# Kernel optimization log

Measured on AMD Instinct MI355X. Metric: run time of the kernel, lower is better.

Reference implementation:

```python
import jax, jax.numpy as jnp
import numpy as np

T, B, D = 2048, 16, 1024
INIT_K_BIAS = -2.0


def setup_inputs() -> dict:
    key = jax.random.key(0)
    k1, k2, k3 = jax.random.split(key, 3)
    xavier = (6.0 / (D + D)) ** 0.5  # xavier_uniform bound for [D, D]
    x = jax.random.normal(k1, (T, B, D), dtype=jnp.float32)
    h0 = jnp.zeros((B, D), dtype=jnp.float32)
    W_k = jax.random.uniform(k2, (D, D), dtype=jnp.float32, minval=-xavier, maxval=xavier)
    b_k = jnp.full((D,), INIT_K_BIAS, dtype=jnp.float32)
    W_v = jax.random.uniform(k3, (D, D), dtype=jnp.float32, minval=-xavier, maxval=xavier)
    b_v = jnp.zeros((D,), dtype=jnp.float32)
    return {"x": x, "h0": h0, "W_k": W_k, "b_k": b_k, "W_v": W_v, "b_v": b_v}


def reference(x, h0, W_k, b_k, W_v, b_v):
    # Batched gate/value projections: x @ W^T + b, over all T*B positions at once.
    k_all = jax.nn.sigmoid(jnp.einsum('tbd,ed->tbe', x, W_k) + b_k)  # [T,B,D]
    v_all = jnp.tanh(jnp.einsum('tbd,ed->tbe', x, W_v) + b_v)        # [T,B,D]

    def step(h_prev, kv):
        k_t, v_t = kv
        h_new = (1.0 - k_t) * h_prev + k_t * v_t
        return h_new, h_new

    _, hs = jax.lax.scan(step, h0, (k_all, v_all))  # hs: [T,B,D]
    h = jnp.concatenate([h0[None], hs], axis=0)      # [T+1,B,D]
    output = hs * jax.nn.silu(hs)                    # [T,B,D]
    return output, h
```

## Files before the change

kernel.cpp:

```cpp
#include <hip/hip_runtime.h>
#include <hip/hip_bf16.h>
#include <stdint.h>
#include <stddef.h>

#define T_DIM 2048
#define B_DIM 16
#define D_DIM 1024
#define BD    (B_DIM * D_DIM)
#define TBD   ((size_t)T_DIM * BD)

using bf16 = __hip_bfloat16;
typedef __attribute__((ext_vector_type(8))) short short8;
typedef __attribute__((ext_vector_type(4))) float f32x4;

__device__ __forceinline__ unsigned f2bf(float f) {
    unsigned u = __float_as_uint(f);
    return (u + 0x7FFFu + ((u >> 16) & 1u)) >> 16;
}

__global__ __launch_bounds__(256) void cvt_f32_bf16(
    const float* __restrict__ src, short* __restrict__ dst, int n8)
{
    int i = blockIdx.x * 256 + threadIdx.x;
    if (i >= n8) return;
    const float* p = src + (size_t)i * 8;
    f32x4 a = *(const f32x4*)p;
    f32x4 b = *(const f32x4*)(p + 4);
    short8 r;
    r[0] = (short)f2bf(a[0]); r[1] = (short)f2bf(a[1]);
    r[2] = (short)f2bf(a[2]); r[3] = (short)f2bf(a[3]);
    r[4] = (short)f2bf(b[0]); r[5] = (short)f2bf(b[1]);
    r[6] = (short)f2bf(b[2]); r[7] = (short)f2bf(b[3]);
    *(short8*)(dst + (size_t)i * 8) = r;
}

typedef __attribute__((address_space(1))) void gvoid;
typedef __attribute__((address_space(3))) void lvoid;
__device__ __forceinline__ void gload_lds16(const short* g, short* l) {
    __builtin_amdgcn_global_load_lds((gvoid*)g, (lvoid*)l, 16, 0, 0);
}

__global__ __launch_bounds__(256, 4) void gemm_kv_bf16(
    const short* __restrict__ xb,
    const short* __restrict__ Wkb, const float* __restrict__ bk,
    const short* __restrict__ Wvb, const float* __restrict__ bv,
    float* __restrict__ kout, float* __restrict__ vout)
{
    __shared__ short sA[2][128 * 32];
    __shared__ short sB[2][128 * 32];

    const int tid  = threadIdx.x;
    const int lane = tid & 63;
    const int wave = tid >> 6;
    const int wm   = wave & 1;
    const int wn   = wave >> 1;
    const int quad = lane >> 4;
    const int l15  = lane & 15;

    const int lin = blockIdx.x + (blockIdx.y << 3) + (blockIdx.z << 11);
    const int swz = ((lin & 7) << 9) | (lin >> 3);
    const bool is_k = (swz >> 11) == 0;
    const int blkm = (swz >> 3) & 255;
    const int blkn = swz & 7;

    const short* W    = is_k ? Wkb : Wvb;
    const float* bias = is_k ? bk : bv;
    float*       outp = is_k ? kout : vout;

    const int m0 = blkm * 128;
    const int n0 = blkn * 128;

    const int srow = wave * 16 + (lane >> 2);
    const int skof = (lane & 3) * 8;
    const short* ga = xb + (size_t)(m0 + srow) * D_DIM + skof;
    const short* gb = W  + (size_t)(n0 + srow) * D_DIM + skof;
    const int lofs = wave * 512;

    auto STAGE = [&](int buf, int ks) {
        const size_t ko = (size_t)ks * 32;
        gload_lds16(ga + ko,                        &sA[buf][lofs]);
        gload_lds16(ga + ko + (size_t)64 * D_DIM,   &sA[buf][2048 + lofs]);
        gload_lds16(gb + ko,                        &sB[buf][lofs]);
        gload_lds16(gb + ko + (size_t)64 * D_DIM,   &sB[buf][2048 + lofs]);
    };

    f32x4 acc[4][4] = {};

    STAGE(0, 0);
    int cur = 0;
    for (int ks = 0; ks < D_DIM / 32; ++ks) {
        __syncthreads();
        if (ks + 1 < D_DIM / 32) STAGE(cur ^ 1, ks + 1);

        const short* lA = sA[cur];
        const short* lB = sB[cur];
        short8 a[4], b[4];
#pragma unroll
        for (int mt = 0; mt < 4; ++mt)
            a[mt] = *(const short8*)&lA[(wm * 64 + mt * 16 + l15) * 32 + quad * 8];
#pragma unroll
        for (int nt = 0; nt < 4; ++nt)
            b[nt] = *(const short8*)&lB[(wn * 64 + nt * 16 + l15) * 32 + quad * 8];
#pragma unroll
        for (int mt = 0; mt < 4; ++mt)
#pragma unroll
            for (int nt = 0; nt < 4; ++nt)
                acc[mt][nt] = __builtin_amdgcn_mfma_f32_16x16x32_bf16(
                    a[mt], b[nt], acc[mt][nt], 0, 0, 0);
        cur ^= 1;
    }

    const int gm0 = blkm * 128 + wm * 64 + quad * 4;
    const int gn  = blkn * 128 + wn * 64 + l15;
#pragma unroll
    for (int nt = 0; nt < 4; ++nt) {
        const int n = gn + nt * 16;
        const float bs = bias[n];
#pragma unroll
        for (int mt = 0; mt < 4; ++mt) {
            const int m = gm0 + mt * 16;
#pragma unroll
            for (int r = 0; r < 4; ++r) {
                float pre = acc[mt][nt][r] + bs;
                pre = fminf(20.f, fmaxf(-20.f, pre));
                float o;
                if (is_k) o = 1.f / (1.f + __expf(-pre));
                else      o = 2.f / (1.f + __expf(-2.f * pre)) - 1.f;
                outp[(size_t)(m + r) * D_DIM + n] = o;
            }
        }
    }
}

__device__ __forceinline__ short8 load_cvt8(const float* p) {
    f32x4 a = *(const f32x4*)p;
    f32x4 b = *(const f32x4*)(p + 4);
    short8 r;
    r[0] = (short)f2bf(a[0]); r[1] = (short)f2bf(a[1]);
    r[2] = (short)f2bf(a[2]); r[3] = (short)f2bf(a[3]);
    r[4] = (short)f2bf(b[0]); r[5] = (short)f2bf(b[1]);
    r[6] = (short)f2bf(b[2]); r[7] = (short)f2bf(b[3]);
    return r;
}

__global__ __launch_bounds__(256) void gemm_kv_f32src(
    const float* __restrict__ x,
    const float* __restrict__ Wk, const float* __restrict__ bk,
    const float* __restrict__ Wv, const float* __restrict__ bv,
    float* __restrict__ kout, float* __restrict__ vout)
{
    const int tid  = threadIdx.x;
    const int lane = tid & 63;
    const int wave = tid >> 6;
    const int wm   = wave & 1;
    const int wn   = wave >> 1;
    const int quad = lane >> 4;
    const int l15  = lane & 15;

    const int blkn = blockIdx.x;
    const int blkm = blockIdx.y;
    const bool is_k = (blockIdx.z == 0);

    const float* W    = is_k ? Wk : Wv;
    const float* bias = is_k ? bk : bv;
    float*       outp = is_k ? kout : vout;

    const int m0 = blkm * 128 + wm * 64;
    const int n0 = blkn * 128 + wn * 64;

    const float* ap = x + (size_t)(m0 + l15) * D_DIM + quad * 8;
    const float* bp = W + (size_t)(n0 + l15) * D_DIM + quad * 8;

    f32x4 acc[4][4] = {};

    for (int ks = 0; ks < D_DIM / 32; ++ks) {
        short8 a[4], b[4];
#pragma unroll
        for (int mt = 0; mt < 4; ++mt)
            a[mt] = load_cvt8(ap + (size_t)mt * 16 * D_DIM + ks * 32);
#pragma unroll
        for (int nt = 0; nt < 4; ++nt)
            b[nt] = load_cvt8(bp + (size_t)nt * 16 * D_DIM + ks * 32);
#pragma unroll
        for (int mt = 0; mt < 4; ++mt)
#pragma unroll
            for (int nt = 0; nt < 4; ++nt)
                acc[mt][nt] = __builtin_amdgcn_mfma_f32_16x16x32_bf16(
                    a[mt], b[nt], acc[mt][nt], 0, 0, 0);
    }

    const int gm0 = blkm * 128 + wm * 64 + quad * 4;
    const int gn  = blkn * 128 + wn * 64 + l15;
#pragma unroll
    for (int nt = 0; nt < 4; ++nt) {
        const int n = gn + nt * 16;
        const float bs = bias[n];
#pragma unroll
        for (int mt = 0; mt < 4; ++mt) {
            const int m = gm0 + mt * 16;
#pragma unroll
            for (int r = 0; r < 4; ++r) {
                float pre = acc[mt][nt][r] + bs;
                pre = fminf(20.f, fmaxf(-20.f, pre));
                float o;
                if (is_k) o = 1.f / (1.f + __expf(-pre));
                else      o = 2.f / (1.f + __expf(-2.f * pre)) - 1.f;
                outp[(size_t)(m + r) * D_DIM + n] = o;
            }
        }
    }
}

__global__ __launch_bounds__(256) void scan_phase_a(
    const float* kw, const float* vw,
    float* __restrict__ Aab, float* __restrict__ Bab, int tc)
{
    const int bd = blockIdx.x * 256 + threadIdx.x;
    const int c  = blockIdx.y;
    const float* kp = kw + (size_t)c * tc * BD + bd;
    const float* vp = vw + (size_t)c * tc * BD + bd;

    float A = 1.f, Bv = 0.f;
    for (int t0 = 0; t0 < tc; t0 += 16) {
        float kk[16], vv[16];
#pragma unroll
        for (int j = 0; j < 16; ++j) {
            kk[j] = kp[(size_t)(t0 + j) * BD];
            vv[j] = vp[(size_t)(t0 + j) * BD];
        }
#pragma unroll
        for (int j = 0; j < 16; ++j) {
            const float a = 1.f - kk[j];
            A  = A * a;
            Bv = a * Bv + kk[j] * vv[j];
        }
    }
    Aab[(size_t)c * BD + bd] = A;
    Bab[(size_t)c * BD + bd] = Bv;
}

__global__ __launch_bounds__(256) void scan_phase_b(
    const float* __restrict__ h0,
    const float* __restrict__ Aab, const float* __restrict__ Bab,
    float* __restrict__ Hinit, float* hsec, int nc)
{
    const int bd = blockIdx.x * 256 + threadIdx.x;
    float h = h0[bd];
    hsec[bd] = h;
    for (int c0 = 0; c0 < nc; c0 += 16) {
        float aa[16], bb[16];
#pragma unroll
        for (int j = 0; j < 16; ++j) {
            aa[j] = Aab[(size_t)(c0 + j) * BD + bd];
            bb[j] = Bab[(size_t)(c0 + j) * BD + bd];
        }
#pragma unroll
        for (int j = 0; j < 16; ++j) {
            Hinit[(size_t)(c0 + j) * BD + bd] = h;
            h = aa[j] * h + bb[j];
        }
    }
}

__global__ __launch_bounds__(256) void scan_phase_c(
    const float* kw, const float* vw, const float* __restrict__ Hinit,
    float* outp, float* hsec, int tc)
{
    const int bd = blockIdx.x * 256 + threadIdx.x;
    const int c  = blockIdx.y;
    float h = Hinit[(size_t)c * BD + bd];

    const size_t base = (size_t)c * tc * BD + bd;
    const float* kp = kw + base;
    const float* vp = vw + base;
    float* op = outp + base;
    float* hp = hsec + base + BD;

    float kk[16], vv[16];
#pragma unroll
    for (int j = 0; j < 16; ++j) {
        kk[j] = kp[(size_t)j * BD];
        vv[j] = vp[(size_t)j * BD];
    }
    for (int t0 = 0; t0 < tc; t0 += 16) {
        float kn[16], vn[16];
        if (t0 + 16 < tc) {
#pragma unroll
            for (int j = 0; j < 16; ++j) {
                kn[j] = kp[(size_t)(t0 + 16 + j) * BD];
                vn[j] = vp[(size_t)(t0 + 16 + j) * BD];
            }
        }
#pragma unroll
        for (int j = 0; j < 16; ++j) {
            h = (1.f - kk[j]) * h + kk[j] * vv[j];
            hp[(size_t)(t0 + j) * BD] = h;
            const float sig = 1.f / (1.f + __expf(-h));
            op[(size_t)(t0 + j) * BD] = h * h * sig;
        }
        if (t0 + 16 < tc) {
#pragma unroll
            for (int j = 0; j < 16; ++j) { kk[j] = kn[j]; vv[j] = vn[j]; }
        }
    }
}

__global__ __launch_bounds__(64) void scan_kernel(
    const float* kw, const float* vw, const float* h0,
    float* outp, float* hsec)
{
    const int c = blockIdx.x * 64 + threadIdx.x;
    float h = h0[c];
    hsec[c] = h;

    const float* kp = kw + c;
    const float* vp = vw + c;
    float* op = outp + c;
    float* hp = hsec + BD + c;

    for (int t = 0; t < T_DIM; t += 8) {
        float kk[8], vv[8];
#pragma unroll
        for (int j = 0; j < 8; ++j) {
            kk[j] = kp[(size_t)(t + j) * BD];
            vv[j] = vp[(size_t)(t + j) * BD];
        }
#pragma unroll
        for (int j = 0; j < 8; ++j) {
            h = (1.f - kk[j]) * h + kk[j] * vv[j];
            hp[(size_t)(t + j) * BD] = h;
            const float sig = 1.f / (1.f + __expf(-h));
            op[(size_t)(t + j) * BD] = h * h * sig;
        }
    }
}

extern "C" void kernel_launch(void* const* d_in, const int* in_sizes, int n_in,
                              void* d_out, int out_size, void* d_ws, size_t ws_size,
                              hipStream_t stream)
{
    const float* x  = (const float*)d_in[0];
    const float* h0 = (const float*)d_in[1];
    const float* Wk = (const float*)d_in[2];
    const float* bk = (const float*)d_in[3];
    const float* Wv = (const float*)d_in[4];
    const float* bv = (const float*)d_in[5];

    float* outp = (float*)d_out;
    float* hsec = outp + TBD;

    float* kw = outp;
    float* vw = hsec + BD;

    const size_t bf16_bytes = (TBD + 2 * (size_t)D_DIM * D_DIM) * sizeof(short);

    bool bf16_path = false;
    size_t avail = ws_size;
    char* scan_ws = (char*)d_ws;
    if (ws_size >= bf16_bytes) {
        bf16_path = true;
        avail   -= bf16_bytes;
        scan_ws += bf16_bytes;
    }

    int nc = 0;
    if (avail >= 3 * (size_t)128 * BD * sizeof(float))      nc = 128;
    else if (avail >= 3 * (size_t)32 * BD * sizeof(float))  nc = 32;
    const int tc = nc ? T_DIM / nc : 0;

    float* Aab   = nc ? (float*)scan_ws : nullptr;
    float* Bab   = nc ? Aab + (size_t)nc * BD : nullptr;
    float* Hinit = nc ? Bab + (size_t)nc * BD : nullptr;

    if (bf16_path) {
        short* xb  = (short*)d_ws;
        short* Wkb = xb + TBD;
        short* Wvb = Wkb + (size_t)D_DIM * D_DIM;
        cvt_f32_bf16<<<dim3((int)(TBD / 8 / 256)), 256, 0, stream>>>(x, xb, (int)(TBD / 8));
        cvt_f32_bf16<<<dim3(D_DIM * D_DIM / 8 / 256), 256, 0, stream>>>(Wk, Wkb, D_DIM * D_DIM / 8);
        cvt_f32_bf16<<<dim3(D_DIM * D_DIM / 8 / 256), 256, 0, stream>>>(Wv, Wvb, D_DIM * D_DIM / 8);
        gemm_kv_bf16<<<dim3(8, 256, 2), 256, 0, stream>>>(xb, Wkb, bk, Wvb, bv, kw, vw);
    } else {
        gemm_kv_f32src<<<dim3(8, 256, 2), 256, 0, stream>>>(x, Wk, bk, Wv, bv, kw, vw);
    }

    if (nc) {
        scan_phase_a<<<dim3(BD / 256, nc), 256, 0, stream>>>(kw, vw, Aab, Bab, tc);
        scan_phase_b<<<dim3(BD / 256), 256, 0, stream>>>(h0, Aab, Bab, Hinit, hsec, nc);
        scan_phase_c<<<dim3(BD / 256, nc), 256, 0, stream>>>(kw, vw, Hinit, outp, hsec, tc);
    } else {
        scan_kernel<<<dim3(BD / 64), 64, 0, stream>>>(kw, vw, h0, outp, hsec);
    }
}
```

Baseline: 702.8 us.

## Fuse K/V GEMMs and compute per-tile scan aggregates in GEMM epilogue

Adds a fused GEMM kernel that computes both the K and V projections per tile, sharing the x tile loads. Its epilogue also reduces each 8-timestep block into (A,B) affine scan aggregates. This removes the separate scan phase A pass that re-read all of k and v from memory, and halves the x reads. A short sequential kernel turns the 256 aggregates into initial states, and a parallel apply kernel produces h and the output. The cost is twice the accumulators per block, so the launch bound drops to 2 blocks per CU and occupancy is lower. The old phase_c prefetch was also simplified.

```diff
diff --git a/kernel.cpp b/kernel.cpp
--- a/kernel.cpp
+++ b/kernel.cpp
@@ -8,6 +8,8 @@
 #define D_DIM 1024
 #define BD    (B_DIM * D_DIM)
 #define TBD   ((size_t)T_DIM * BD)
+#define NG    256
+#define TG    8
 
 using bf16 = __hip_bfloat16;
 typedef __attribute__((ext_vector_type(8))) short short8;
@@ -40,14 +42,25 @@
     __builtin_amdgcn_global_load_lds((gvoid*)g, (lvoid*)l, 16, 0, 0);
 }
 
-__global__ __launch_bounds__(256, 4) void gemm_kv_bf16(
+__device__ __forceinline__ float sigm(float x) {
+    x = fminf(20.f, fmaxf(-20.f, x));
+    return 1.f / (1.f + __expf(-x));
+}
+__device__ __forceinline__ float tanh_(float x) {
+    x = fminf(20.f, fmaxf(-20.f, x));
+    return 2.f / (1.f + __expf(-2.f * x)) - 1.f;
+}
+
+__global__ __launch_bounds__(256, 2) void gemm_kv_fused(
     const short* __restrict__ xb,
     const short* __restrict__ Wkb, const float* __restrict__ bk,
     const short* __restrict__ Wvb, const float* __restrict__ bv,
-    float* __restrict__ kout, float* __restrict__ vout)
+    float* __restrict__ kout, float* __restrict__ vout,
+    float2* __restrict__ agg)
 {
     __shared__ short sA[2][128 * 32];
-    __shared__ short sB[2][128 * 32];
+    __shared__ short sBk[2][128 * 32];
+    __shared__ short sBv[2][128 * 32];
 
     const int tid  = threadIdx.x;
     const int lane = tid & 63;
@@ -57,6 +70,132 @@
     const int quad = lane >> 4;
     const int l15  = lane & 15;
 
+    const int lin = blockIdx.x + (blockIdx.y << 3);
+    const int swz = ((lin & 7) << 8) | (lin >> 3);
+    const int blkm = swz >> 3;
+    const int blkn = swz & 7;
+
+    const int m0 = blkm * 128;
+    const int n0 = blkn * 128;
+
+    const int srow = wave * 16 + (lane >> 2);
+    const int skof = (lane & 3) * 8;
+    const short* ga = xb  + (size_t)(m0 + srow) * D_DIM + skof;
+    const short* gk = Wkb + (size_t)(n0 + srow) * D_DIM + skof;
+    const short* gv = Wvb + (size_t)(n0 + srow) * D_DIM + skof;
+    const int lofs = wave * 512;
+
+    auto STAGE = [&](int buf, int ks) {
+        const size_t ko = (size_t)ks * 32;
+        gload_lds16(ga + ko,                        &sA[buf][lofs]);
+        gload_lds16(ga + ko + (size_t)64 * D_DIM,   &sA[buf][2048 + lofs]);
+        gload_lds16(gk + ko,                        &sBk[buf][lofs]);
+        gload_lds16(gk + ko + (size_t)64 * D_DIM,   &sBk[buf][2048 + lofs]);
+        gload_lds16(gv + ko,                        &sBv[buf][lofs]);
+        gload_lds16(gv + ko + (size_t)64 * D_DIM,   &sBv[buf][2048 + lofs]);
+    };
+
+    f32x4 ack[4][4] = {};
+    f32x4 acv[4][4] = {};
+
+    STAGE(0, 0);
+    int cur = 0;
+    for (int ks = 0; ks < D_DIM / 32; ++ks) {
+        __syncthreads();
+        if (ks + 1 < D_DIM / 32) STAGE(cur ^ 1, ks + 1);
+
+        const short* lA = sA[cur];
+        const short* lK = sBk[cur];
+        const short* lV = sBv[cur];
+        short8 a[4], bkf[4], bvf[4];
+#pragma unroll
+        for (int mt = 0; mt < 4; ++mt)
+            a[mt] = *(const short8*)&lA[(wm * 64 + mt * 16 + l15) * 32 + quad * 8];
+#pragma unroll
+        for (int nt = 0; nt < 4; ++nt) {
+            bkf[nt] = *(const short8*)&lK[(wn * 64 + nt * 16 + l15) * 32 + quad * 8];
+            bvf[nt] = *(const short8*)&lV[(wn * 64 + nt * 16 + l15) * 32 + quad * 8];
+        }
+#pragma unroll
+        for (int mt = 0; mt < 4; ++mt)
+#pragma unroll
+            for (int nt = 0; nt < 4; ++nt) {
+                ack[mt][nt] = __builtin_amdgcn_mfma_f32_16x16x32_bf16(
+                    a[mt], bkf[nt], ack[mt][nt], 0, 0, 0);
+                acv[mt][nt] = __builtin_amdgcn_mfma_f32_16x16x32_bf16(
+                    a[mt], bvf[nt], acv[mt][nt], 0, 0, 0);
+            }
+        cur ^= 1;
+    }
+
+    const int gm0 = blkm * 128 + wm * 64 + quad * 4;
+    const int gn  = n0 + wn * 64 + l15;
+    float2 part[4][4];
+#pragma unroll
+    for (int nt = 0; nt < 4; ++nt) {
+        const int n = gn + nt * 16;
+        const float bks = bk[n];
+        const float bvs = bv[n];
+#pragma unroll
+        for (int r = 0; r < 4; ++r) {
+            float A = 1.f, Bv = 0.f;
+#pragma unroll
+            for (int mt = 0; mt < 4; ++mt) {
+                const int m = gm0 + mt * 16 + r;
+                const float ke = sigm(ack[mt][nt][r] + bks);
+                const float ve = tanh_(acv[mt][nt][r] + bvs);
+                kout[(size_t)m * D_DIM + n] = ke;
+                vout[(size_t)m * D_DIM + n] = ve;
+                const float a1 = 1.f - ke;
+                Bv = a1 * Bv + ke * ve;
+                A *= a1;
+            }
+            part[nt][r] = make_float2(A, Bv);
+        }
+    }
+
+    __syncthreads();
+    float2* lp = (float2*)sA;
+    if (wm == 1) {
+#pragma unroll
+        for (int nt = 0; nt < 4; ++nt)
+#pragma unroll
+            for (int r = 0; r < 4; ++r)
+                lp[(quad * 4 + r) * 128 + wn * 64 + nt * 16 + l15] = part[nt][r];
+    }
+    __syncthreads();
+    if (wm == 0) {
+#pragma unroll
+        for (int nt = 0; nt < 4; ++nt)
+#pragma unroll
+            for (int r = 0; r < 4; ++r) {
+                const int b = quad * 4 + r;
+                const int d = n0 + wn * 64 + nt * 16 + l15;
+                const float2 hi = lp[b * 128 + wn * 64 + nt * 16 + l15];
+                const float A8 = hi.x * part[nt][r].x;
+                const float B8 = hi.x * part[nt][r].y + hi.y;
+                agg[(size_t)blkm * BD + b * D_DIM + d] = make_float2(A8, B8);
+            }
+    }
+}
+
+__global__ __launch_bounds__(256, 4) void gemm_kv_bf16(
+    const short* __restrict__ xb,
+    const short* __restrict__ Wkb, const float* __restrict__ bk,
+    const short* __restrict__ Wvb, const float* __restrict__ bv,
+    float* __restrict__ kout, float* __restrict__ vout)
+{
+    __shared__ short sA[2][128 * 32];
+    __shared__ short sB[2][128 * 32];
+
+    const int tid  = threadIdx.x;
+    const int lane = tid & 63;
+    const int wave = tid >> 6;
+    const int wm   = wave & 1;
+    const int wn   = wave >> 1;
+    const int quad = lane >> 4;
+    const int l15  = lane & 15;
+
     const int lin = blockIdx.x + (blockIdx.y << 3) + (blockIdx.z << 11);
     const int swz = ((lin & 7) << 9) | (lin >> 3);
     const bool is_k = (swz >> 11) == 0;
@@ -78,10 +217,10 @@
 
     auto STAGE = [&](int buf, int ks) {
         const size_t ko = (size_t)ks * 32;
-        gload_lds16(ga + ko,                        &sA[buf][lofs]);
-        gload_lds16(ga + ko + (size_t)64 * D_DIM,   &sA[buf][2048 + lofs]);
-        gload_lds16(gb + ko,                        &sB[buf][lofs]);
-        gload_lds16(gb + ko + (size_t)64 * D_DIM,   &sB[buf][2048 + lofs]);
+        gload_lds16(ga + ko,                      &sA[buf][lofs]);
+        gload_lds16(ga + ko + (size_t)64 * D_DIM, &sA[buf][2048 + lofs]);
+        gload_lds16(gb + ko,                      &sB[buf][lofs]);
+        gload_lds16(gb + ko + (size_t)64 * D_DIM, &sB[buf][2048 + lofs]);
     };
 
     f32x4 acc[4][4] = {};
@@ -121,12 +260,8 @@
             const int m = gm0 + mt * 16;
 #pragma unroll
             for (int r = 0; r < 4; ++r) {
-                float pre = acc[mt][nt][r] + bs;
-                pre = fminf(20.f, fmaxf(-20.f, pre));
-                float o;
-                if (is_k) o = 1.f / (1.f + __expf(-pre));
-                else      o = 2.f / (1.f + __expf(-2.f * pre)) - 1.f;
-                outp[(size_t)(m + r) * D_DIM + n] = o;
+                const float pre = acc[mt][nt][r] + bs;
+                outp[(size_t)(m + r) * D_DIM + n] = is_k ? sigm(pre) : tanh_(pre);
             }
         }
     }
@@ -200,14 +335,58 @@
             const int m = gm0 + mt * 16;
 #pragma unroll
             for (int r = 0; r < 4; ++r) {
-                float pre = acc[mt][nt][r] + bs;
-                pre = fminf(20.f, fmaxf(-20.f, pre));
-                float o;
-                if (is_k) o = 1.f / (1.f + __expf(-pre));
-                else      o = 2.f / (1.f + __expf(-2.f * pre)) - 1.f;
-                outp[(size_t)(m + r) * D_DIM + n] = o;
+                const float pre = acc[mt][nt][r] + bs;
+                outp[(size_t)(m + r) * D_DIM + n] = is_k ? sigm(pre) : tanh_(pre);
             }
         }
+    }
+}
+
+__global__ __launch_bounds__(256) void scan_hinit(
+    const float* __restrict__ h0, float2* agg, float* hsec)
+{
+    const int ch = blockIdx.x * 256 + threadIdx.x;
+    float h = h0[ch];
+    hsec[ch] = h;
+    for (int g0 = 0; g0 < NG; g0 += 16) {
+        float2 ag[16];
+#pragma unroll
+        for (int j = 0; j < 16; ++j)
+            ag[j] = agg[(size_t)(g0 + j) * BD + ch];
+#pragma unroll
+        for (int j = 0; j < 16; ++j) {
+            agg[(size_t)(g0 + j) * BD + ch].x = h;
+            h = ag[j].x * h + ag[j].y;
+        }
+    }
+}
+
+__global__ __launch_bounds__(256) void scan_apply(
+    const float* kw, const float* vw, const float2* __restrict__ agg,
+    float* outp, float* hsec)
+{
+    const int ch = blockIdx.x * 256 + threadIdx.x;
+    const int tg = blockIdx.y;
+    float h = agg[(size_t)tg * BD + ch].x;
+
+    const size_t base = (size_t)tg * TG * BD + ch;
+    const float* kp = kw + base;
+    const float* vp = vw + base;
+    float* op = outp + base;
+    float* hp = hsec + base + BD;
+
+    float kk[TG], vv[TG];
+#pragma unroll
+    for (int j = 0; j < TG; ++j) {
+        kk[j] = kp[(size_t)j * BD];
+        vv[j] = vp[(size_t)j * BD];
+    }
+#pragma unroll
+    for (int j = 0; j < TG; ++j) {
+        h = (1.f - kk[j]) * h + kk[j] * vv[j];
+        hp[(size_t)j * BD] = h;
+        const float sig = 1.f / (1.f + __expf(-h));
+        op[(size_t)j * BD] = h * h * sig;
     }
 }
 
@@ -276,20 +455,12 @@
     float* op = outp + base;
     float* hp = hsec + base + BD;
 
-    float kk[16], vv[16];
-#pragma unroll
-    for (int j = 0; j < 16; ++j) {
-        kk[j] = kp[(size_t)j * BD];
-        vv[j] = vp[(size_t)j * BD];
-    }
     for (int t0 = 0; t0 < tc; t0 += 16) {
-        float kn[16], vn[16];
-        if (t0 + 16 < tc) {
-#pragma unroll
-            for (int j = 0; j < 16; ++j) {
-                kn[j] = kp[(size_t)(t0 + 16 + j) * BD];
-                vn[j] = vp[(size_t)(t0 + 16 + j) * BD];
-            }
+        float kk[16], vv[16];
+#pragma unroll
+        for (int j = 0; j < 16; ++j) {
+            kk[j] = kp[(size_t)(t0 + j) * BD];
+            vv[j] = vp[(size_t)(t0 + j) * BD];
         }
 #pragma unroll
         for (int j = 0; j < 16; ++j) {
@@ -297,10 +468,6 @@
             hp[(size_t)(t0 + j) * BD] = h;
             const float sig = 1.f / (1.f + __expf(-h));
             op[(size_t)(t0 + j) * BD] = h * h * sig;
-        }
-        if (t0 + 16 < tc) {
-#pragma unroll
-            for (int j = 0; j < 16; ++j) { kk[j] = kn[j]; vv[j] = vn[j]; }
         }
     }
 }
@@ -353,6 +520,7 @@
     float* vw = hsec + BD;
 
     const size_t bf16_bytes = (TBD + 2 * (size_t)D_DIM * D_DIM) * sizeof(short);
+    const size_t agg_bytes  = (size_t)NG * BD * sizeof(float2);
 
     bool bf16_path = false;
     size_t avail = ws_size;
@@ -363,14 +531,10 @@
         scan_ws += bf16_bytes;
     }
 
-    int nc = 0;
-    if (avail >= 3 * (size_t)128 * BD * sizeof(float))      nc = 128;
-    else if (avail >= 3 * (size_t)32 * BD * sizeof(float))  nc = 32;
-    const int tc = nc ? T_DIM / nc : 0;
-
-    float* Aab   = nc ? (float*)scan_ws : nullptr;
-    float* Bab   = nc ? Aab + (size_t)nc * BD : nullptr;
-    float* Hinit = nc ? Bab + (size_t)nc * BD : nullptr;
+    int mode = 0, nc = 0;
+    if (bf16_path && avail >= agg_bytes) mode = 2;
+    else if (avail >= 3 * (size_t)128 * BD * sizeof(float)) { mode = 1; nc = 128; }
+    else if (avail >= 3 * (size_t)32  * BD * sizeof(float)) { mode = 1; nc = 32; }
 
     if (bf16_path) {
         short* xb  = (short*)d_ws;
@@ -379,12 +543,24 @@
         cvt_f32_bf16<<<dim3((int)(TBD / 8 / 256)), 256, 0, stream>>>(x, xb, (int)(TBD / 8));
         cvt_f32_bf16<<<dim3(D_DIM * D_DIM / 8 / 256), 256, 0, stream>>>(Wk, Wkb, D_DIM * D_DIM / 8);
         cvt_f32_bf16<<<dim3(D_DIM * D_DIM / 8 / 256), 256, 0, stream>>>(Wv, Wvb, D_DIM * D_DIM / 8);
+        if (mode == 2) {
+            float2* agg = (float2*)scan_ws;
+            gemm_kv_fused<<<dim3(8, 256), 256, 0, stream>>>(
+                xb, Wkb, bk, Wvb, bv, kw, vw, agg);
+            scan_hinit<<<dim3(BD / 256), 256, 0, stream>>>(h0, agg, hsec);
+            scan_apply<<<dim3(BD / 256, NG), 256, 0, stream>>>(kw, vw, agg, outp, hsec);
+            return;
+        }
         gemm_kv_bf16<<<dim3(8, 256, 2), 256, 0, stream>>>(xb, Wkb, bk, Wvb, bv, kw, vw);
     } else {
         gemm_kv_f32src<<<dim3(8, 256, 2), 256, 0, stream>>>(x, Wk, bk, Wv, bv, kw, vw);
     }
 
-    if (nc) {
+    if (mode == 1) {
+        const int tc = T_DIM / nc;
+        float* Aab   = (float*)scan_ws;
+        float* Bab   = Aab + (size_t)nc * BD;
+        float* Hinit = Bab + (size_t)nc * BD;
         scan_phase_a<<<dim3(BD / 256, nc), 256, 0, stream>>>(kw, vw, Aab, Bab, tc);
         scan_phase_b<<<dim3(BD / 256), 256, 0, stream>>>(h0, Aab, Bab, Hinit, hsec, nc);
         scan_phase_c<<<dim3(BD / 256, nc), 256, 0, stream>>>(kw, vw, Hinit, outp, hsec, tc);
```

Measured after the change: 707.8 us. About the same (+0.7%).
